# Performance work log

Hardware: AMD Instinct MI355X
Metric: run time of the kernel (lower is better)

## Reference

```python
import jax, jax.numpy as jnp
import numpy as np

N, E, IN_DIM, D, T, L, B, SLEN, C = 50000, 600000, 128, 128, 4, 2, 2048, 16, 16


def _deg_inv_sqrt(idx, n, dtype):
    deg = jax.ops.segment_sum(jnp.ones(idx.shape, dtype=dtype), idx, num_segments=n)
    return jnp.where(deg > 0, deg ** -0.5, 0.0).astype(dtype)


def gcn_conv(h, edge_index, W, b):
    # PyG GCNConv: add self loops, symmetric norm, x@W, scatter-add, +bias
    n = h.shape[0]
    loop = jnp.arange(n)
    row = jnp.concatenate([edge_index[0], loop])
    col = jnp.concatenate([edge_index[1], loop])
    dis = _deg_inv_sqrt(col, n, h.dtype)
    norm = dis[row] * dis[col]              # [E+N]
    xw = h @ W                               # [N, D]
    msgs = xw[row] * norm[:, None]           # [E+N, D] gather
    out = jax.ops.segment_sum(msgs, col, num_segments=n)
    return out + b


def re_conv(r, edge_index, node_type, W, wtype, b):
    # REConv(norm='both'): left-norm by src out-degree, x@W, type weight,
    # scatter-add to dst, right-norm by dst in-degree, +bias, relu
    n = r.shape[0]
    row, col = edge_index
    dl = _deg_inv_sqrt(row, n, r.dtype)
    x = (r * dl[:, None]) @ W                # [N, T]
    x = x * wtype[node_type][:, None]
    out = jax.ops.segment_sum(x[row], col, num_segments=n)
    dr = _deg_inv_sqrt(col, n, r.dtype)
    out = out * dr[:, None] + b
    return jax.nn.relu(out)


def setup_inputs() -> dict:
    key = jax.random.key(0)
    ks = jax.random.split(key, 10)
    x = jax.random.normal(ks[0], (N, IN_DIM), dtype=jnp.float32)
    label = jax.random.randint(ks[1], (N,), 0, C)
    seqs = jax.random.randint(ks[2], (B, SLEN), 0, N)
    edge_index = jax.random.randint(ks[3], (2, E), 0, N)
    node_type = jnp.sort(jax.random.randint(ks[4], (N,), 0, T))
    s_in = 1.0 / np.sqrt(IN_DIM)
    s_d = 1.0 / np.sqrt(D)
    fcW = jax.random.normal(ks[5], (T, IN_DIM, D), dtype=jnp.float32) * s_in
    fcB = jnp.zeros((T, D), dtype=jnp.float32)
    gcnW = jax.random.normal(ks[6], (L, D, D), dtype=jnp.float32) * s_d
    gcnB = jnp.zeros((L, D), dtype=jnp.float32)
    reW = jax.random.normal(ks[7], (L, T, T), dtype=jnp.float32) * 0.5
    re_wtype = jnp.ones((L, T), dtype=jnp.float32)
    reB = jnp.zeros((L, T), dtype=jnp.float32)
    predW = jax.random.normal(ks[8], (D, C), dtype=jnp.float32) * s_d
    predB = jnp.zeros((C,), dtype=jnp.float32)
    return {"x": x, "label": label, "seqs": seqs, "edge_index": edge_index,
            "node_type": node_type, "fcW": fcW, "fcB": fcB, "gcnW": gcnW,
            "gcnB": gcnB, "reW": reW, "re_wtype": re_wtype, "reB": reB,
            "predW": predW, "predB": predB}


def reference(x, label, seqs, edge_index, node_type, fcW, fcB, gcnW, gcnB,
              reW, re_wtype, reB, predW, predB):
    n = x.shape[0]
    # per-type input projection; node_type is sorted so this equals
    # torch.cat([fc[t](x[node_type==t]) for t])
    h_all = jnp.einsum('ni,tio->tno', x, fcW) + fcB[:, None, :]  # [T, N, D]
    gh = h_all[node_type, jnp.arange(n)]                          # [N, D]
    r = jnp.eye(fcW.shape[0], dtype=x.dtype)[node_type]           # [N, T]
    for l in range(gcnW.shape[0]):
        gh = jax.nn.relu(gcn_conv(gh, edge_index, gcnW[l], gcnB[l]))
        r = re_conv(r, edge_index, node_type, reW[l], re_wtype[l], reB[l])
    ego = seqs[:, 0]
    output = gh[ego] @ predW + predB                               # [B, C]
    return output, label[ego]
```

## Files before the change

### kernel.cpp

```cpp
#include <hip/hip_runtime.h>
#include <hip/hip_bf16.h>


typedef __attribute__((ext_vector_type(8))) short short8;
typedef __attribute__((ext_vector_type(4))) float f32x4;
typedef unsigned short u16;

__device__ __forceinline__ float bf2f(u16 u) {
  union { float f; unsigned int i; } v; v.i = (unsigned int)u << 16; return v.f;
}
__device__ __forceinline__ u16 f2bf(float f) {
  union { float f; unsigned int i; } v; v.f = f;
  return (u16)((v.i + 0x7FFF + ((v.i >> 16) & 1)) >> 16);
}

#define NPB 128
#define SWZ(row, byte) ((byte) ^ (((row) & 15) << 4))

__global__ void k_prep(const float* __restrict__ fcW, const float* __restrict__ gcnW,
                       u16* __restrict__ wt, int* __restrict__ ecnt,
                       int* __restrict__ cnt, int T, int wt_total, int n) {
  const int gt = blockIdx.x * 256 + threadIdx.x;
  const int GT = gridDim.x * 256;
  for (int i = gt; i < wt_total; i += GT) {
    int m = i >> 14, dk = i & 16383, d = dk >> 7, k = dk & 127;
    const float* src = (m < T) ? (fcW + ((size_t)m << 14)) : (gcnW + ((size_t)(m - T) << 14));
    wt[i] = f2bf(src[k * 128 + d]);
  }
  for (int i = gt; i < n; i += GT) ecnt[i] = 0;
  if (gt == 0) *cnt = 0;
}

__device__ __forceinline__ void stage_tile_bf16(char* smem, const u16* __restrict__ gsrc,
                                                int rows_valid, int t) {
  int row = t >> 1;
  int h = (t & 1) * 64;
  int byte0 = row * 256 + h * 2;
  if (row < rows_valid) {
    const u16* src = gsrc + (size_t)row * 128 + h;
#pragma unroll
    for (int j = 0; j < 8; ++j) {
      short8 v = *(const short8*)(src + j * 8);
      *(short8*)(smem + SWZ(row, byte0 + j * 16)) = v;
    }
  } else {
    short8 z = (short8){0, 0, 0, 0, 0, 0, 0, 0};
#pragma unroll
    for (int j = 0; j < 8; ++j)
      *(short8*)(smem + SWZ(row, byte0 + j * 16)) = z;
  }
}

__device__ __forceinline__ void mfma_core128_g(const char* xs, const u16* __restrict__ wtg,
                                               int t, f32x4 acc[8][2]) {
  const int lane = t & 63, w = t >> 6;
  const int lr = lane & 15, lk = lane >> 4;
  short8 bfrag[4][2];
#pragma unroll
  for (int ks = 0; ks < 4; ++ks)
#pragma unroll
    for (int ch = 0; ch < 2; ++ch) {
      int row = w * 32 + ch * 16 + lr;
      bfrag[ks][ch] = *(const short8*)(wtg + (size_t)row * 128 + ks * 32 + lk * 8);
    }
#pragma unroll
  for (int ks = 0; ks < 4; ++ks) {
    int kb = ks * 64 + lk * 16;
    short8 a[8];
#pragma unroll
    for (int rg = 0; rg < 8; ++rg) {
      int row = rg * 16 + lr;
      a[rg] = *(const short8*)(xs + SWZ(row, row * 256 + kb));
    }
#pragma unroll
    for (int rg = 0; rg < 8; ++rg)
#pragma unroll
      for (int ch = 0; ch < 2; ++ch)
        acc[rg][ch] = __builtin_amdgcn_mfma_f32_16x16x32_bf16(a[rg], bfrag[ks][ch],
                                                              acc[rg][ch], 0, 0, 0);
  }
}

__global__ __launch_bounds__(256) void k_fc(const float* __restrict__ x,
                                            const int* __restrict__ node_type,
                                            const u16* __restrict__ wt_fc,
                                            const float* __restrict__ fcB,
                                            u16* __restrict__ gh, int n_nodes,
                                            const int* __restrict__ col,
                                            int* __restrict__ ecnt, int e_edges) {
  __shared__ char smem_xs[32768];
  const int t = threadIdx.x;
  const int nbase = blockIdx.x * NPB;
  const int nend = min(nbase + NPB, n_nodes);
  const int t0 = node_type[nbase];
  const int t1 = node_type[nend - 1];

  {
    int row = t >> 1;
    int h = (t & 1) * 64;
    int node = nbase + row;
    int byte0 = row * 256 + h * 2;
    if (node < n_nodes) {
      const float4* src = (const float4*)(x + (size_t)node * 128 + h);
#pragma unroll
      for (int j = 0; j < 8; ++j) {
        float4 a4 = src[j * 2], b4 = src[j * 2 + 1];
        u16 tmp[8] = {f2bf(a4.x), f2bf(a4.y), f2bf(a4.z), f2bf(a4.w),
                      f2bf(b4.x), f2bf(b4.y), f2bf(b4.z), f2bf(b4.w)};
        *(short8*)(smem_xs + SWZ(row, byte0 + j * 16)) = *(short8*)tmp;
      }
    } else {
      short8 z = (short8){0, 0, 0, 0, 0, 0, 0, 0};
#pragma unroll
      for (int j = 0; j < 8; ++j)
        *(short8*)(smem_xs + SWZ(row, byte0 + j * 16)) = z;
    }
  }
  __syncthreads();

  const int lane = t & 63, w = t >> 6;
  const int lr = lane & 15, lk = lane >> 4;

  for (int tt = t0; tt <= t1; ++tt) {
    f32x4 acc[8][2];
#pragma unroll
    for (int rg = 0; rg < 8; ++rg)
#pragma unroll
      for (int ch = 0; ch < 2; ++ch) acc[rg][ch] = (f32x4){0.f, 0.f, 0.f, 0.f};
    mfma_core128_g(smem_xs, wt_fc + ((size_t)tt << 14), t, acc);

    float bv0 = fcB[tt * 128 + w * 32 + lr];
    float bv1 = fcB[tt * 128 + w * 32 + 16 + lr];
#pragma unroll
    for (int rg = 0; rg < 8; ++rg) {
#pragma unroll
      for (int reg = 0; reg < 4; ++reg) {
        int node = nbase + rg * 16 + lk * 4 + reg;
        if (node < n_nodes && node_type[node] == tt) {
          gh[(size_t)node * 128 + w * 32 + lr]      = f2bf(acc[rg][0][reg] + bv0);
          gh[(size_t)node * 128 + w * 32 + 16 + lr] = f2bf(acc[rg][1][reg] + bv1);
        }
      }
    }
  }

  const int gt = blockIdx.x * 256 + t;
  const int GT = gridDim.x * 256;
  for (int i = gt; i < e_edges; i += GT) atomicAdd(&ecnt[col[i]], 1);
}

__global__ __launch_bounds__(256) void k_gemm_scale(const u16* __restrict__ ghin,
                                                    const u16* __restrict__ wtg,
                                                    const float* __restrict__ dis,
                                                    u16* __restrict__ xws, int n_nodes,
                                                    const int* __restrict__ row,
                                                    const int* __restrict__ col,
                                                    int* __restrict__ cursor,
                                                    int* __restrict__ edge_row,
                                                    int e_edges, int do_fill) {
  __shared__ char smem_xs[32768];
  const int t = threadIdx.x;
  const int nbase = blockIdx.x * NPB;

  stage_tile_bf16(smem_xs, ghin + (size_t)nbase * 128, min(n_nodes - nbase, NPB), t);
  __syncthreads();

  f32x4 acc[8][2];
#pragma unroll
  for (int rg = 0; rg < 8; ++rg)
#pragma unroll
    for (int ch = 0; ch < 2; ++ch) acc[rg][ch] = (f32x4){0.f, 0.f, 0.f, 0.f};
  mfma_core128_g(smem_xs, wtg, t, acc);

  const int lane = t & 63, w = t >> 6;
  const int lr = lane & 15, lk = lane >> 4;
#pragma unroll
  for (int rg = 0; rg < 8; ++rg) {
#pragma unroll
    for (int reg = 0; reg < 4; ++reg) {
      int node = nbase + rg * 16 + lk * 4 + reg;
      if (node < n_nodes) {
        float s = dis[node];
        xws[(size_t)node * 128 + w * 32 + lr]      = f2bf(acc[rg][0][reg] * s);
        xws[(size_t)node * 128 + w * 32 + 16 + lr] = f2bf(acc[rg][1][reg] * s);
      }
    }
  }

  if (do_fill) {
    const int gt = blockIdx.x * 256 + t;
    const int GT = gridDim.x * 256;
    for (int i = gt; i < e_edges; i += GT) {
      int c = col[i];
      int pos = atomicAdd(&cursor[c], 1);
      edge_row[pos] = row[i];
    }
  }
}

__global__ __launch_bounds__(256) void k_scan1(const int* __restrict__ ecnt,
                                               int* __restrict__ scanex,
                                               int* __restrict__ partials,
                                               float* __restrict__ dis,
                                               int* __restrict__ cnt, int n) {
  __shared__ int s[256];
  __shared__ int lastflag;
  const int t = threadIdx.x;
  const int i = blockIdx.x * 256 + t;
  int v = (i < n) ? ecnt[i] : 0;
  s[t] = v;
  __syncthreads();
  for (int off = 1; off < 256; off <<= 1) {
    int add = (t >= off) ? s[t - off] : 0;
    __syncthreads();
    s[t] += add;
    __syncthreads();
  }
  if (i < n) {
    scanex[i] = s[t] - v;
    dis[i] = rsqrtf((float)(v + 1));
  }
  if (t == 255) partials[blockIdx.x] = s[t];
  __threadfence();
  if (t == 0) lastflag = (atomicAdd(cnt, 1) == gridDim.x - 1) ? 1 : 0;
  __syncthreads();
  if (lastflag) {
    __threadfence();
    int np = gridDim.x;
    int pv = (t < np) ? partials[t] : 0;
    s[t] = pv;
    __syncthreads();
    for (int off = 1; off < 256; off <<= 1) {
      int add = (t >= off) ? s[t - off] : 0;
      __syncthreads();
      s[t] += add;
      __syncthreads();
    }
    if (t < np) partials[t] = s[t] - pv;
  }
}

__global__ void k_scan3(const int* __restrict__ scanex, const int* __restrict__ partials,
                        int* __restrict__ col_ptr, int* __restrict__ cursor,
                        int n, int e_total) {
  int i = blockIdx.x * 256 + threadIdx.x;
  if (i < n) {
    int p = scanex[i] + partials[i >> 8];
    col_ptr[i] = p;
    cursor[i] = p;
  }
  if (i == 0) col_ptr[n] = e_total;
}

__device__ __forceinline__ void gather_node(int node, const int* __restrict__ col_ptr,
                                            const int* __restrict__ edge_row,
                                            const u16* __restrict__ xws,
                                            const float* __restrict__ dis,
                                            const float* __restrict__ bias,
                                            u16* __restrict__ dst, int lane) {
  const int g = lane & 15;
  const int s = lane >> 4;
  float acc[8] = {0.f, 0.f, 0.f, 0.f, 0.f, 0.f, 0.f, 0.f};
  if (s == 0) {
    short8 v = *(const short8*)(xws + (size_t)node * 128 + g * 8);
#pragma unroll
    for (int j = 0; j < 8; ++j) acc[j] = bf2f((u16)v[j]);
  }
  const int e0 = col_ptr[node], e1 = col_ptr[node + 1];
  for (int e = e0 + s; e < e1; e += 4) {
    int r = edge_row[e];
    short8 v = *(const short8*)(xws + (size_t)r * 128 + g * 8);
#pragma unroll
    for (int j = 0; j < 8; ++j) acc[j] += bf2f((u16)v[j]);
  }
#pragma unroll
  for (int j = 0; j < 8; ++j) {
    acc[j] += __shfl_xor(acc[j], 16);
    acc[j] += __shfl_xor(acc[j], 32);
  }
  if (s == 0) {
    float ds = dis[node];
    u16 o[8];
#pragma unroll
    for (int j = 0; j < 8; ++j)
      o[j] = f2bf(fmaxf(acc[j] * ds + bias[g * 8 + j], 0.f));
    *(short8*)(dst + g * 8) = *(short8*)o;
  }
}

__global__ __launch_bounds__(256) void k_gather(const int* __restrict__ col_ptr,
                                                const int* __restrict__ edge_row,
                                                const u16* __restrict__ xws,
                                                const float* __restrict__ dis,
                                                const float* __restrict__ bias,
                                                u16* __restrict__ gh, int n_nodes) {
  const int t = threadIdx.x;
  const int node = blockIdx.x * 4 + (t >> 6);
  if (node >= n_nodes) return;
  gather_node(node, col_ptr, edge_row, xws, dis, bias,
              gh + (size_t)node * 128, t & 63);
}

__global__ __launch_bounds__(256) void k_egopred(const int* __restrict__ col_ptr,
                                                 const int* __restrict__ edge_row,
                                                 const u16* __restrict__ xws,
                                                 const float* __restrict__ dis,
                                                 const float* __restrict__ bias,
                                                 const int* __restrict__ seqs,
                                                 const int* __restrict__ label,
                                                 const float* __restrict__ predW,
                                                 const float* __restrict__ predB,
                                                 float* __restrict__ out,
                                                 float* __restrict__ out_label,
                                                 int b_total, int n_classes, int slen) {
  __shared__ u16 buf[4][128];
  const int t = threadIdx.x;
  const int w = t >> 6, lane = t & 63;
  const int b = blockIdx.x * 4 + w;
  int node = -1;
  if (b < b_total) {
    node = seqs[(size_t)b * slen];
    gather_node(node, col_ptr, edge_row, xws, dis, bias, &buf[w][0], lane);
  }
  __syncthreads();
  if (b < b_total) {
    const int c = lane & 15;
    const int q = lane >> 4;
    float s = 0.f;
#pragma unroll 8
    for (int k = q * 32; k < q * 32 + 32; ++k)
      s += bf2f(buf[w][k]) * predW[k * n_classes + c];
    s += __shfl_xor(s, 16);
    s += __shfl_xor(s, 32);
    if (q == 0) out[(size_t)b * n_classes + c] = s + predB[c];
    if (lane == 0) out_label[b] = (float)label[node];
  }
}

extern "C" void kernel_launch(void* const* d_in, const int* in_sizes, int n_in,
                              void* d_out, int out_size, void* d_ws, size_t ws_size,
                              hipStream_t stream) {
  const float* x     = (const float*)d_in[0];
  const int*   label = (const int*)d_in[1];
  const int*   seqs  = (const int*)d_in[2];
  const int*   edge  = (const int*)d_in[3];
  const int*   ntype = (const int*)d_in[4];
  const float* fcW   = (const float*)d_in[5];
  const float* fcB   = (const float*)d_in[6];
  const float* gcnW  = (const float*)d_in[7];
  const float* gcnB  = (const float*)d_in[8];
  const float* predW = (const float*)d_in[12];
  const float* predB = (const float*)d_in[13];

  const int n = in_sizes[0] / 128;
  const int e = in_sizes[3] / 2;
  const int T = in_sizes[5] / (128 * 128);
  const int L = in_sizes[8] / 128;
  const int C = in_sizes[13];
  const int slen = 16;
  const int b_total = in_sizes[2] / slen;

  const int* row = edge;
  const int* col = edge + e;

  char* ws = (char*)d_ws;
  const size_t node_bf = (size_t)n * 128 * sizeof(u16);
  u16*   gh      = (u16*)ws;                 ws += node_bf;
  u16*   xws     = (u16*)ws;                 ws += node_bf;
  u16*   wt      = (u16*)ws;                 ws += (size_t)(T + L) * 16384 * 2;
  float* dis     = (float*)ws;               ws += (size_t)n * 4;
  int*   ecnt    = (int*)ws;                 ws += (size_t)n * 4;
  int*   scanex  = (int*)ws;                 ws += (size_t)n * 4;
  int*   col_ptr = (int*)ws;                 ws += (size_t)(n + 16) * 4;
  int*   cursor  = (int*)ws;                 ws += (size_t)n * 4;
  int*   partial = (int*)ws;                 ws += 1024 * 4;
  int*   cnt     = (int*)ws;                 ws += 64;
  int*   edge_row= (int*)ws;                 ws += (size_t)e * 4;

  float* out_logits = (float*)d_out;
  float* out_label  = out_logits + (size_t)b_total * C;

  const int nb = (n + NPB - 1) / NPB;
  const int nscan = (n + 255) / 256;
  const int wt_total = (T + L) * 16384;

  hipLaunchKernelGGL(k_prep, dim3(384), dim3(256), 0, stream,
                     fcW, gcnW, wt, ecnt, cnt, T, wt_total, n);
  hipLaunchKernelGGL(k_fc, dim3(nb), dim3(256), 0, stream,
                     x, ntype, wt, fcB, gh, n, col, ecnt, e);
  hipLaunchKernelGGL(k_scan1, dim3(nscan), dim3(256), 0, stream,
                     ecnt, scanex, partial, dis, cnt, n);
  hipLaunchKernelGGL(k_scan3, dim3(nscan), dim3(256), 0, stream,
                     scanex, partial, col_ptr, cursor, n, e);

  for (int l = 0; l < L; ++l) {
    hipLaunchKernelGGL(k_gemm_scale, dim3(nb), dim3(256), 0, stream,
                       gh, wt + (size_t)(T + l) * 16384, dis, xws, n,
                       row, col, cursor, edge_row, e, (l == 0) ? 1 : 0);
    if (l < L - 1) {
      hipLaunchKernelGGL(k_gather, dim3((n + 3) / 4), dim3(256), 0, stream,
                         col_ptr, edge_row, xws, dis, gcnB + (size_t)l * 128, gh, n);
    } else {
      hipLaunchKernelGGL(k_egopred, dim3((b_total + 3) / 4), dim3(256), 0, stream,
                         col_ptr, edge_row, xws, dis, gcnB + (size_t)l * 128,
                         seqs, label, predW, predB, out_logits, out_label,
                         b_total, C, slen);
    }
  }
}
```

Measured before the change: 256.5 us.

## Aggregate before transform and run last-layer GEMM only on ego nodes

Reorders each GCN layer to gather-then-multiply (A·(XW) = (A·X)·W), so the last layer's aggregation and GEMM run only for the ego batch rows instead of all nodes. It also moves the CSR fill out of the first GEMM kernel into the scan3 kernel, and stages weights in shared memory for the MFMA cores. This removes a full-graph GEMM and a full-graph gather in the final layer. The trade-off is that the number of layers is now hardcoded to two, and shared memory per block doubles, which may reduce occupancy.

```diff
diff --git a/kernel.cpp b/kernel.cpp
--- a/kernel.cpp
+++ b/kernel.cpp
@@ -19,7 +19,8 @@
 
 __global__ void k_prep(const float* __restrict__ fcW, const float* __restrict__ gcnW,
                        u16* __restrict__ wt, int* __restrict__ ecnt,
-                       int* __restrict__ cnt, int T, int wt_total, int n) {
+                       int* __restrict__ slot, int* __restrict__ cnt,
+                       int T, int wt_total, int n) {
   const int gt = blockIdx.x * 256 + threadIdx.x;
   const int GT = gridDim.x * 256;
   for (int i = gt; i < wt_total; i += GT) {
@@ -27,7 +28,7 @@
     const float* src = (m < T) ? (fcW + ((size_t)m << 14)) : (gcnW + ((size_t)(m - T) << 14));
     wt[i] = f2bf(src[k * 128 + d]);
   }
-  for (int i = gt; i < n; i += GT) ecnt[i] = 0;
+  for (int i = gt; i < n; i += GT) { ecnt[i] = 0; slot[i] = 0; }
   if (gt == 0) *cnt = 0;
 }
 
@@ -51,18 +52,20 @@
   }
 }
 
-__device__ __forceinline__ void mfma_core128_g(const char* xs, const u16* __restrict__ wtg,
-                                               int t, f32x4 acc[8][2]) {
+__device__ __forceinline__ void mfma_core128(const char* xs, const char* wt, int t,
+                                             f32x4 acc[8][2]) {
   const int lane = t & 63, w = t >> 6;
   const int lr = lane & 15, lk = lane >> 4;
   short8 bfrag[4][2];
 #pragma unroll
-  for (int ks = 0; ks < 4; ++ks)
+  for (int ks = 0; ks < 4; ++ks) {
+    int kb = ks * 64 + lk * 16;
 #pragma unroll
     for (int ch = 0; ch < 2; ++ch) {
       int row = w * 32 + ch * 16 + lr;
-      bfrag[ks][ch] = *(const short8*)(wtg + (size_t)row * 128 + ks * 32 + lk * 8);
-    }
+      bfrag[ks][ch] = *(const short8*)(wt + SWZ(row, row * 256 + kb));
+    }
+  }
 #pragma unroll
   for (int ks = 0; ks < 4; ++ks) {
     int kb = ks * 64 + lk * 16;
@@ -88,7 +91,9 @@
                                             u16* __restrict__ gh, int n_nodes,
                                             const int* __restrict__ col,
                                             int* __restrict__ ecnt, int e_edges) {
-  __shared__ char smem_xs[32768];
+  __shared__ char smem[65536];
+  char* smem_xs = smem;
+  char* smem_wt = smem + 32768;
   const int t = threadIdx.x;
   const int nbase = blockIdx.x * NPB;
   const int nend = min(nbase + NPB, n_nodes);
@@ -116,18 +121,21 @@
         *(short8*)(smem_xs + SWZ(row, byte0 + j * 16)) = z;
     }
   }
-  __syncthreads();
 
   const int lane = t & 63, w = t >> 6;
   const int lr = lane & 15, lk = lane >> 4;
 
   for (int tt = t0; tt <= t1; ++tt) {
+    __syncthreads();
+    stage_tile_bf16(smem_wt, wt_fc + ((size_t)tt << 14), 128, t);
+    __syncthreads();
+
     f32x4 acc[8][2];
 #pragma unroll
     for (int rg = 0; rg < 8; ++rg)
 #pragma unroll
       for (int ch = 0; ch < 2; ++ch) acc[rg][ch] = (f32x4){0.f, 0.f, 0.f, 0.f};
-    mfma_core128_g(smem_xs, wt_fc + ((size_t)tt << 14), t, acc);
+    mfma_core128(smem_xs, smem_wt, t, acc);
 
     float bv0 = fcB[tt * 128 + w * 32 + lr];
     float bv1 = fcB[tt * 128 + w * 32 + 16 + lr];
@@ -147,55 +155,6 @@
   const int gt = blockIdx.x * 256 + t;
   const int GT = gridDim.x * 256;
   for (int i = gt; i < e_edges; i += GT) atomicAdd(&ecnt[col[i]], 1);
-}
-
-__global__ __launch_bounds__(256) void k_gemm_scale(const u16* __restrict__ ghin,
-                                                    const u16* __restrict__ wtg,
-                                                    const float* __restrict__ dis,
-                                                    u16* __restrict__ xws, int n_nodes,
-                                                    const int* __restrict__ row,
-                                                    const int* __restrict__ col,
-                                                    int* __restrict__ cursor,
-                                                    int* __restrict__ edge_row,
-                                                    int e_edges, int do_fill) {
-  __shared__ char smem_xs[32768];
-  const int t = threadIdx.x;
-  const int nbase = blockIdx.x * NPB;
-
-  stage_tile_bf16(smem_xs, ghin + (size_t)nbase * 128, min(n_nodes - nbase, NPB), t);
-  __syncthreads();
-
-  f32x4 acc[8][2];
-#pragma unroll
-  for (int rg = 0; rg < 8; ++rg)
-#pragma unroll
-    for (int ch = 0; ch < 2; ++ch) acc[rg][ch] = (f32x4){0.f, 0.f, 0.f, 0.f};
-  mfma_core128_g(smem_xs, wtg, t, acc);
-
-  const int lane = t & 63, w = t >> 6;
-  const int lr = lane & 15, lk = lane >> 4;
-#pragma unroll
-  for (int rg = 0; rg < 8; ++rg) {
-#pragma unroll
-    for (int reg = 0; reg < 4; ++reg) {
-      int node = nbase + rg * 16 + lk * 4 + reg;
-      if (node < n_nodes) {
-        float s = dis[node];
-        xws[(size_t)node * 128 + w * 32 + lr]      = f2bf(acc[rg][0][reg] * s);
-        xws[(size_t)node * 128 + w * 32 + 16 + lr] = f2bf(acc[rg][1][reg] * s);
-      }
-    }
-  }
-
-  if (do_fill) {
-    const int gt = blockIdx.x * 256 + t;
-    const int GT = gridDim.x * 256;
-    for (int i = gt; i < e_edges; i += GT) {
-      int c = col[i];
-      int pos = atomicAdd(&cursor[c], 1);
-      edge_row[pos] = row[i];
-    }
-  }
 }
 
 __global__ __launch_bounds__(256) void k_scan1(const int* __restrict__ ecnt,
@@ -240,38 +199,44 @@
   }
 }
 
-__global__ void k_scan3(const int* __restrict__ scanex, const int* __restrict__ partials,
-                        int* __restrict__ col_ptr, int* __restrict__ cursor,
-                        int n, int e_total) {
-  int i = blockIdx.x * 256 + threadIdx.x;
-  if (i < n) {
-    int p = scanex[i] + partials[i >> 8];
-    col_ptr[i] = p;
-    cursor[i] = p;
-  }
-  if (i == 0) col_ptr[n] = e_total;
-}
-
-__device__ __forceinline__ void gather_node(int node, const int* __restrict__ col_ptr,
-                                            const int* __restrict__ edge_row,
-                                            const u16* __restrict__ xws,
-                                            const float* __restrict__ dis,
-                                            const float* __restrict__ bias,
-                                            u16* __restrict__ dst, int lane) {
+__global__ void k_scan3_fill(const int* __restrict__ scanex,
+                             const int* __restrict__ partials,
+                             int* __restrict__ col_ptr, int* __restrict__ slot,
+                             const int* __restrict__ row, const int* __restrict__ col,
+                             int* __restrict__ edge_row, int n, int e_total) {
+  const int gt = blockIdx.x * 256 + threadIdx.x;
+  const int GT = gridDim.x * 256;
+  if (gt < n) col_ptr[gt] = scanex[gt] + partials[gt >> 8];
+  if (gt == 0) col_ptr[n] = e_total;
+  for (int i = gt; i < e_total; i += GT) {
+    int c = col[i];
+    int base = scanex[c] + partials[c >> 8];
+    int pos = base + atomicAdd(&slot[c], 1);
+    edge_row[pos] = row[i];
+  }
+}
+
+__device__ __forceinline__ void gather_s(int node, const int* __restrict__ col_ptr,
+                                         const int* __restrict__ edge_row,
+                                         const u16* __restrict__ gh,
+                                         const float* __restrict__ dis,
+                                         u16* __restrict__ dst, int lane) {
   const int g = lane & 15;
   const int s = lane >> 4;
   float acc[8] = {0.f, 0.f, 0.f, 0.f, 0.f, 0.f, 0.f, 0.f};
   if (s == 0) {
-    short8 v = *(const short8*)(xws + (size_t)node * 128 + g * 8);
-#pragma unroll
-    for (int j = 0; j < 8; ++j) acc[j] = bf2f((u16)v[j]);
+    float ds = dis[node];
+    short8 v = *(const short8*)(gh + (size_t)node * 128 + g * 8);
+#pragma unroll
+    for (int j = 0; j < 8; ++j) acc[j] = bf2f((u16)v[j]) * ds;
   }
   const int e0 = col_ptr[node], e1 = col_ptr[node + 1];
   for (int e = e0 + s; e < e1; e += 4) {
     int r = edge_row[e];
-    short8 v = *(const short8*)(xws + (size_t)r * 128 + g * 8);
-#pragma unroll
-    for (int j = 0; j < 8; ++j) acc[j] += bf2f((u16)v[j]);
+    float dr = dis[r];
+    short8 v = *(const short8*)(gh + (size_t)r * 128 + g * 8);
+#pragma unroll
+    for (int j = 0; j < 8; ++j) acc[j] += bf2f((u16)v[j]) * dr;
   }
 #pragma unroll
   for (int j = 0; j < 8; ++j) {
@@ -279,61 +244,170 @@
     acc[j] += __shfl_xor(acc[j], 32);
   }
   if (s == 0) {
-    float ds = dis[node];
     u16 o[8];
 #pragma unroll
-    for (int j = 0; j < 8; ++j)
-      o[j] = f2bf(fmaxf(acc[j] * ds + bias[g * 8 + j], 0.f));
+    for (int j = 0; j < 8; ++j) o[j] = f2bf(acc[j]);
     *(short8*)(dst + g * 8) = *(short8*)o;
   }
 }
 
 __global__ __launch_bounds__(256) void k_gather(const int* __restrict__ col_ptr,
                                                 const int* __restrict__ edge_row,
-                                                const u16* __restrict__ xws,
+                                                const u16* __restrict__ gh,
                                                 const float* __restrict__ dis,
-                                                const float* __restrict__ bias,
-                                                u16* __restrict__ gh, int n_nodes) {
+                                                u16* __restrict__ agg, int n_nodes) {
   const int t = threadIdx.x;
   const int node = blockIdx.x * 4 + (t >> 6);
   if (node >= n_nodes) return;
-  gather_node(node, col_ptr, edge_row, xws, dis, bias,
-              gh + (size_t)node * 128, t & 63);
-}
-
-__global__ __launch_bounds__(256) void k_egopred(const int* __restrict__ col_ptr,
-                                                 const int* __restrict__ edge_row,
-                                                 const u16* __restrict__ xws,
-                                                 const float* __restrict__ dis,
-                                                 const float* __restrict__ bias,
-                                                 const int* __restrict__ seqs,
-                                                 const int* __restrict__ label,
-                                                 const float* __restrict__ predW,
-                                                 const float* __restrict__ predB,
-                                                 float* __restrict__ out,
-                                                 float* __restrict__ out_label,
-                                                 int b_total, int n_classes, int slen) {
-  __shared__ u16 buf[4][128];
-  const int t = threadIdx.x;
-  const int w = t >> 6, lane = t & 63;
-  const int b = blockIdx.x * 4 + w;
-  int node = -1;
-  if (b < b_total) {
-    node = seqs[(size_t)b * slen];
-    gather_node(node, col_ptr, edge_row, xws, dis, bias, &buf[w][0], lane);
-  }
+  gather_s(node, col_ptr, edge_row, gh, dis, agg + (size_t)node * 128, t & 63);
+}
+
+__global__ __launch_bounds__(256) void k_gather_ego(const int* __restrict__ col_ptr,
+                                                    const int* __restrict__ edge_row,
+                                                    const u16* __restrict__ gh,
+                                                    const float* __restrict__ dis,
+                                                    const int* __restrict__ seqs,
+                                                    u16* __restrict__ agg2,
+                                                    int b_total, int slen) {
+  const int t = threadIdx.x;
+  const int b = blockIdx.x * 4 + (t >> 6);
+  if (b >= b_total) return;
+  int node = seqs[(size_t)b * slen];
+  gather_s(node, col_ptr, edge_row, gh, dis, agg2 + (size_t)b * 128, t & 63);
+}
+
+__global__ __launch_bounds__(256) void k_gemm(const u16* __restrict__ agg,
+                                              const u16* __restrict__ wtg,
+                                              const float* __restrict__ dis,
+                                              const float* __restrict__ bias,
+                                              u16* __restrict__ gh, int n_nodes) {
+  __shared__ char smem[65536];
+  char* smem_xs = smem;
+  char* smem_wt = smem + 32768;
+  const int t = threadIdx.x;
+  const int nbase = blockIdx.x * NPB;
+
+  stage_tile_bf16(smem_xs, agg + (size_t)nbase * 128, min(n_nodes - nbase, NPB), t);
+  stage_tile_bf16(smem_wt, wtg, 128, t);
   __syncthreads();
-  if (b < b_total) {
-    const int c = lane & 15;
-    const int q = lane >> 4;
-    float s = 0.f;
+
+  f32x4 acc[8][2];
+#pragma unroll
+  for (int rg = 0; rg < 8; ++rg)
+#pragma unroll
+    for (int ch = 0; ch < 2; ++ch) acc[rg][ch] = (f32x4){0.f, 0.f, 0.f, 0.f};
+  mfma_core128(smem_xs, smem_wt, t, acc);
+
+  const int lane = t & 63, w = t >> 6;
+  const int lr = lane & 15, lk = lane >> 4;
+  float bv0 = bias[w * 32 + lr];
+  float bv1 = bias[w * 32 + 16 + lr];
+#pragma unroll
+  for (int rg = 0; rg < 8; ++rg) {
+#pragma unroll
+    for (int reg = 0; reg < 4; ++reg) {
+      int node = nbase + rg * 16 + lk * 4 + reg;
+      if (node < n_nodes) {
+        float s = dis[node];
+        gh[(size_t)node * 128 + w * 32 + lr] =
+            f2bf(fmaxf(acc[rg][0][reg] * s + bv0, 0.f));
+        gh[(size_t)node * 128 + w * 32 + 16 + lr] =
+            f2bf(fmaxf(acc[rg][1][reg] * s + bv1, 0.f));
+      }
+    }
+  }
+}
+
+__global__ __launch_bounds__(256) void k_tail(const u16* __restrict__ agg2,
+                                              const u16* __restrict__ wt1,
+                                              const float* __restrict__ dis,
+                                              const float* __restrict__ bias,
+                                              const int* __restrict__ seqs,
+                                              const int* __restrict__ label,
+                                              const float* __restrict__ predW,
+                                              const float* __restrict__ predB,
+                                              float* __restrict__ out,
+                                              float* __restrict__ out_label,
+                                              int b_total, int n_classes, int slen) {
+  __shared__ char smem_wt[32768];
+  __shared__ char smem_xs[8192];
+  __shared__ u16 gh2[32 * 128];
+  __shared__ int egos[32];
+  const int t = threadIdx.x;
+  const int b0 = blockIdx.x * 32;
+
+  stage_tile_bf16(smem_wt, wt1, 128, t);
+  {
+    int row = t >> 3;
+    int h = (t & 7) * 8;
+    int bb = b0 + row;
+    short8 v;
+    if (bb < b_total) v = *(const short8*)(agg2 + (size_t)bb * 128 + h);
+    else v = (short8){0, 0, 0, 0, 0, 0, 0, 0};
+    *(short8*)(smem_xs + SWZ(row, row * 256 + h * 2)) = v;
+  }
+  if (t < 32) egos[t] = (b0 + t < b_total) ? seqs[(size_t)(b0 + t) * slen] : 0;
+  __syncthreads();
+
+  const int lane = t & 63, w = t >> 6;
+  const int lr = lane & 15, lk = lane >> 4;
+  f32x4 acc[2][2];
+#pragma unroll
+  for (int rg = 0; rg < 2; ++rg)
+#pragma unroll
+    for (int ch = 0; ch < 2; ++ch) acc[rg][ch] = (f32x4){0.f, 0.f, 0.f, 0.f};
+  {
+    short8 bfrag[4][2];
+#pragma unroll
+    for (int ks = 0; ks < 4; ++ks) {
+      int kb = ks * 64 + lk * 16;
+#pragma unroll
+      for (int ch = 0; ch < 2; ++ch) {
+        int rowb = w * 32 + ch * 16 + lr;
+        bfrag[ks][ch] = *(const short8*)(smem_wt + SWZ(rowb, rowb * 256 + kb));
+      }
+    }
+#pragma unroll
+    for (int ks = 0; ks < 4; ++ks) {
+      int kb = ks * 64 + lk * 16;
+      short8 a[2];
+#pragma unroll
+      for (int rg = 0; rg < 2; ++rg) {
+        int row = rg * 16 + lr;
+        a[rg] = *(const short8*)(smem_xs + SWZ(row, row * 256 + kb));
+      }
+#pragma unroll
+      for (int rg = 0; rg < 2; ++rg)
+#pragma unroll
+        for (int ch = 0; ch < 2; ++ch)
+          acc[rg][ch] = __builtin_amdgcn_mfma_f32_16x16x32_bf16(a[rg], bfrag[ks][ch],
+                                                                acc[rg][ch], 0, 0, 0);
+    }
+  }
+#pragma unroll
+  for (int rg = 0; rg < 2; ++rg) {
+#pragma unroll
+    for (int reg = 0; reg < 4; ++reg) {
+      int row = rg * 16 + lk * 4 + reg;
+      float s = dis[egos[row]];
+#pragma unroll
+      for (int ch = 0; ch < 2; ++ch) {
+        int dout = w * 32 + ch * 16 + lr;
+        gh2[row * 128 + dout] = f2bf(fmaxf(acc[rg][ch][reg] * s + bias[dout], 0.f));
+      }
+    }
+  }
+  __syncthreads();
+
+  for (int idx = t; idx < 32 * n_classes; idx += 256) {
+    int row = idx / n_classes, c = idx - (idx / n_classes) * n_classes;
+    if (b0 + row >= b_total) continue;
+    float s = predB[c];
 #pragma unroll 8
-    for (int k = q * 32; k < q * 32 + 32; ++k)
-      s += bf2f(buf[w][k]) * predW[k * n_classes + c];
-    s += __shfl_xor(s, 16);
-    s += __shfl_xor(s, 32);
-    if (q == 0) out[(size_t)b * n_classes + c] = s + predB[c];
-    if (lane == 0) out_label[b] = (float)label[node];
+    for (int k = 0; k < 128; ++k)
+      s += bf2f(gh2[row * 128 + k]) * predW[k * n_classes + c];
+    out[(size_t)(b0 + row) * n_classes + c] = s;
+    if (c == 0) out_label[b0 + row] = (float)label[egos[row]];
   }
 }
 
@@ -355,7 +429,6 @@
   const int n = in_sizes[0] / 128;
   const int e = in_sizes[3] / 2;
   const int T = in_sizes[5] / (128 * 128);
-  const int L = in_sizes[8] / 128;
   const int C = in_sizes[13];
   const int slen = 16;
   const int b_total = in_sizes[2] / slen;
@@ -366,13 +439,14 @@
   char* ws = (char*)d_ws;
   const size_t node_bf = (size_t)n * 128 * sizeof(u16);
   u16*   gh      = (u16*)ws;                 ws += node_bf;
-  u16*   xws     = (u16*)ws;                 ws += node_bf;
-  u16*   wt      = (u16*)ws;                 ws += (size_t)(T + L) * 16384 * 2;
+  u16*   agg     = (u16*)ws;                 ws += node_bf;
+  u16*   agg2    = (u16*)ws;                 ws += (size_t)b_total * 128 * 2;
+  u16*   wt      = (u16*)ws;                 ws += (size_t)(T + 2) * 16384 * 2;
   float* dis     = (float*)ws;               ws += (size_t)n * 4;
   int*   ecnt    = (int*)ws;                 ws += (size_t)n * 4;
   int*   scanex  = (int*)ws;                 ws += (size_t)n * 4;
   int*   col_ptr = (int*)ws;                 ws += (size_t)(n + 16) * 4;
-  int*   cursor  = (int*)ws;                 ws += (size_t)n * 4;
+  int*   slot    = (int*)ws;                 ws += (size_t)n * 4;
   int*   partial = (int*)ws;                 ws += 1024 * 4;
   int*   cnt     = (int*)ws;                 ws += 64;
   int*   edge_row= (int*)ws;                 ws += (size_t)e * 4;
@@ -382,29 +456,26 @@
 
   const int nb = (n + NPB - 1) / NPB;
   const int nscan = (n + 255) / 256;
-  const int wt_total = (T + L) * 16384;
+  const int wt_total = (T + 2) * 16384;
 
   hipLaunchKernelGGL(k_prep, dim3(384), dim3(256), 0, stream,
-                     fcW, gcnW, wt, ecnt, cnt, T, wt_total, n);
+                     fcW, gcnW, wt, ecnt, slot, cnt, T, wt_total, n);
   hipLaunchKernelGGL(k_fc, dim3(nb), dim3(256), 0, stream,
                      x, ntype, wt, fcB, gh, n, col, ecnt, e);
   hipLaunchKernelGGL(k_scan1, dim3(nscan), dim3(256), 0, stream,
                      ecnt, scanex, partial, dis, cnt, n);
-  hipLaunchKernelGGL(k_scan3, dim3(nscan), dim3(256), 0, stream,
-                     scanex, partial, col_ptr, cursor, n, e);
-
-  for (int l = 0; l < L; ++l) {
-    hipLaunchKernelGGL(k_gemm_scale, dim3(nb), dim3(256), 0, stream,
-                       gh, wt + (size_t)(T + l) * 16384, dis, xws, n,
-                       row, col, cursor, edge_row, e, (l == 0) ? 1 : 0);
-    if (l < L - 1) {
-      hipLaunchKernelGGL(k_gather, dim3((n + 3) / 4), dim3(256), 0, stream,
-                         col_ptr, edge_row, xws, dis, gcnB + (size_t)l * 128, gh, n);
-    } else {
-      hipLaunchKernelGGL(k_egopred, dim3((b_total + 3) / 4), dim3(256), 0, stream,
-                         col_ptr, edge_row, xws, dis, gcnB + (size_t)l * 128,
-                         seqs, label, predW, predB, out_logits, out_label,
-                         b_total, C, slen);
-    }
-  }
-}
+  hipLaunchKernelGGL(k_scan3_fill, dim3(1024), dim3(256), 0, stream,
+                     scanex, partial, col_ptr, slot, row, col, edge_row, n, e);
+
+  hipLaunchKernelGGL(k_gather, dim3((n + 3) / 4), dim3(256), 0, stream,
+                     col_ptr, edge_row, gh, dis, agg, n);
+  hipLaunchKernelGGL(k_gemm, dim3(nb), dim3(256), 0, stream,
+                     agg, wt + (size_t)T * 16384, dis, gcnB, gh, n);
+
+  hipLaunchKernelGGL(k_gather_ego, dim3((b_total + 3) / 4), dim3(256), 0, stream,
+                     col_ptr, edge_row, gh, dis, seqs, agg2, b_total, slen);
+  hipLaunchKernelGGL(k_tail, dim3((b_total + 31) / 32), dim3(256), 0, stream,
+                     agg2, wt + (size_t)(T + 1) * 16384, dis, gcnB + 128,
+                     seqs, label, predW, predB, out_logits, out_label,
+                     b_total, C, slen);
+}
```

Result: faster. 251.1 us (-2.1%).

## Stage weights in LDS and coalesce GEMM output stores through shared memory

Applied to the files above, without the earlier changes.

The FC and GCN GEMM kernels now copy the bf16 weight tile into swizzled shared memory before the MFMA loop instead of loading B fragments straight from global memory. Results are first written into LDS, then each thread stores full 128-byte row segments, replacing the scattered 2-byte global stores. This aims at better store coalescing and cheaper weight-fragment loads. In exchange it doubles LDS per block to 64 KB, which may lower occupancy, and adds extra barriers. The dis float4 load reads past n_nodes on the last tile unless the buffer is padded.

```diff
diff --git a/kernel.cpp b/kernel.cpp
--- a/kernel.cpp
+++ b/kernel.cpp
@@ -51,18 +51,20 @@
   }
 }
 
-__device__ __forceinline__ void mfma_core128_g(const char* xs, const u16* __restrict__ wtg,
-                                               int t, f32x4 acc[8][2]) {
+__device__ __forceinline__ void mfma_core128(const char* xs, const char* wt, int t,
+                                             f32x4 acc[8][2]) {
   const int lane = t & 63, w = t >> 6;
   const int lr = lane & 15, lk = lane >> 4;
   short8 bfrag[4][2];
 #pragma unroll
-  for (int ks = 0; ks < 4; ++ks)
+  for (int ks = 0; ks < 4; ++ks) {
+    int kb = ks * 64 + lk * 16;
 #pragma unroll
     for (int ch = 0; ch < 2; ++ch) {
       int row = w * 32 + ch * 16 + lr;
-      bfrag[ks][ch] = *(const short8*)(wtg + (size_t)row * 128 + ks * 32 + lk * 8);
-    }
+      bfrag[ks][ch] = *(const short8*)(wt + SWZ(row, row * 256 + kb));
+    }
+  }
 #pragma unroll
   for (int ks = 0; ks < 4; ++ks) {
     int kb = ks * 64 + lk * 16;
@@ -88,7 +90,9 @@
                                             u16* __restrict__ gh, int n_nodes,
                                             const int* __restrict__ col,
                                             int* __restrict__ ecnt, int e_edges) {
-  __shared__ char smem_xs[32768];
+  __shared__ char smem[65536];
+  char* smem_xs = smem;
+  char* smem_wt = smem + 32768;
   const int t = threadIdx.x;
   const int nbase = blockIdx.x * NPB;
   const int nend = min(nbase + NPB, n_nodes);
@@ -116,30 +120,46 @@
         *(short8*)(smem_xs + SWZ(row, byte0 + j * 16)) = z;
     }
   }
-  __syncthreads();
 
   const int lane = t & 63, w = t >> 6;
   const int lr = lane & 15, lk = lane >> 4;
 
   for (int tt = t0; tt <= t1; ++tt) {
+    __syncthreads();
+    stage_tile_bf16(smem_wt, wt_fc + ((size_t)tt << 14), 128, t);
+    __syncthreads();
+
     f32x4 acc[8][2];
 #pragma unroll
     for (int rg = 0; rg < 8; ++rg)
 #pragma unroll
       for (int ch = 0; ch < 2; ++ch) acc[rg][ch] = (f32x4){0.f, 0.f, 0.f, 0.f};
-    mfma_core128_g(smem_xs, wt_fc + ((size_t)tt << 14), t, acc);
-
+    mfma_core128(smem_xs, smem_wt, t, acc);
+
+    __syncthreads();
+    u16* tb = (u16*)smem_wt;
     float bv0 = fcB[tt * 128 + w * 32 + lr];
     float bv1 = fcB[tt * 128 + w * 32 + 16 + lr];
 #pragma unroll
     for (int rg = 0; rg < 8; ++rg) {
 #pragma unroll
       for (int reg = 0; reg < 4; ++reg) {
-        int node = nbase + rg * 16 + lk * 4 + reg;
-        if (node < n_nodes && node_type[node] == tt) {
-          gh[(size_t)node * 128 + w * 32 + lr]      = f2bf(acc[rg][0][reg] + bv0);
-          gh[(size_t)node * 128 + w * 32 + 16 + lr] = f2bf(acc[rg][1][reg] + bv1);
-        }
+        int row = rg * 16 + lk * 4 + reg;
+        tb[row * 128 + w * 32 + lr]      = f2bf(acc[rg][0][reg] + bv0);
+        tb[row * 128 + w * 32 + 16 + lr] = f2bf(acc[rg][1][reg] + bv1);
+      }
+    }
+    __syncthreads();
+    {
+      int row = t >> 1;
+      int h = (t & 1) * 64;
+      int node = nbase + row;
+      if (node < n_nodes && node_type[node] == tt) {
+        u16* dst = gh + (size_t)node * 128 + h;
+        const u16* srcp = tb + row * 128 + h;
+#pragma unroll
+        for (int j = 0; j < 8; ++j)
+          *(short8*)(dst + j * 8) = *(const short8*)(srcp + j * 8);
       }
     }
   }
@@ -158,11 +178,14 @@
                                                     int* __restrict__ cursor,
                                                     int* __restrict__ edge_row,
                                                     int e_edges, int do_fill) {
-  __shared__ char smem_xs[32768];
+  __shared__ char smem[65536];
+  char* smem_xs = smem;
+  char* smem_wt = smem + 32768;
   const int t = threadIdx.x;
   const int nbase = blockIdx.x * NPB;
 
   stage_tile_bf16(smem_xs, ghin + (size_t)nbase * 128, min(n_nodes - nbase, NPB), t);
+  stage_tile_bf16(smem_wt, wtg, 128, t);
   __syncthreads();
 
   f32x4 acc[8][2];
@@ -170,20 +193,35 @@
   for (int rg = 0; rg < 8; ++rg)
 #pragma unroll
     for (int ch = 0; ch < 2; ++ch) acc[rg][ch] = (f32x4){0.f, 0.f, 0.f, 0.f};
-  mfma_core128_g(smem_xs, wtg, t, acc);
+  mfma_core128(smem_xs, smem_wt, t, acc);
 
   const int lane = t & 63, w = t >> 6;
   const int lr = lane & 15, lk = lane >> 4;
+
+  __syncthreads();
+  u16* tb = (u16*)smem_wt;
 #pragma unroll
   for (int rg = 0; rg < 8; ++rg) {
+    float4 d4 = *(const float4*)(dis + nbase + rg * 16 + lk * 4);
 #pragma unroll
     for (int reg = 0; reg < 4; ++reg) {
-      int node = nbase + rg * 16 + lk * 4 + reg;
-      if (node < n_nodes) {
-        float s = dis[node];
-        xws[(size_t)node * 128 + w * 32 + lr]      = f2bf(acc[rg][0][reg] * s);
-        xws[(size_t)node * 128 + w * 32 + 16 + lr] = f2bf(acc[rg][1][reg] * s);
-      }
+      float dv = (&d4.x)[reg];
+      int row = rg * 16 + lk * 4 + reg;
+      tb[row * 128 + w * 32 + lr]      = f2bf(acc[rg][0][reg] * dv);
+      tb[row * 128 + w * 32 + 16 + lr] = f2bf(acc[rg][1][reg] * dv);
+    }
+  }
+  __syncthreads();
+  {
+    int rowi = t >> 1;
+    int h = (t & 1) * 64;
+    int node = nbase + rowi;
+    if (node < n_nodes) {
+      u16* dst = xws + (size_t)node * 128 + h;
+      const u16* srcp = tb + rowi * 128 + h;
+#pragma unroll
+      for (int j = 0; j < 8; ++j)
+        *(short8*)(dst + j * 8) = *(const short8*)(srcp + j * 8);
     }
   }
 
```

After: 243.4 us. 1.05x faster.
